# Kernel tuning notes

Hardware: AMD Instinct MI355X
Metric: run time of the kernel (lower is better)

The kernel has to match this reference:

```python
import jax, jax.numpy as jnp
import numpy as np

B, N, DA, DB = 8, 2048, 768, 1024


def setup_inputs() -> dict:
    key = jax.random.key(0)
    ks = jax.random.split(key, 20)
    s = 0.02
    inp = {
        "x_a": jax.random.normal(ks[0], (B, N, DA), jnp.float32),
        "x_b": jax.random.normal(ks[1], (B, N, DB), jnp.float32),
        # self-attention params (all DB x DB), stored as [in, out]
        "sa_wq": jax.random.normal(ks[2], (DB, DB), jnp.float32) * s,
        "sa_bq": jnp.zeros((DB,), jnp.float32),
        "sa_wk": jax.random.normal(ks[3], (DB, DB), jnp.float32) * s,
        "sa_bk": jnp.zeros((DB,), jnp.float32),
        "sa_wv": jax.random.normal(ks[4], (DB, DB), jnp.float32) * s,
        "sa_bv": jnp.zeros((DB,), jnp.float32),
        "sa_wo": jax.random.normal(ks[5], (DB, DB), jnp.float32) * s,
        "sa_bo": jnp.zeros((DB,), jnp.float32),
        # cross-attention params: q maps DA->DB, rest DB->DB
        "ca_wq": jax.random.normal(ks[6], (DA, DB), jnp.float32) * s,
        "ca_bq": jnp.zeros((DB,), jnp.float32),
        "ca_wk": jax.random.normal(ks[7], (DB, DB), jnp.float32) * s,
        "ca_bk": jnp.zeros((DB,), jnp.float32),
        "ca_wv": jax.random.normal(ks[8], (DB, DB), jnp.float32) * s,
        "ca_bv": jnp.zeros((DB,), jnp.float32),
        "ca_wo": jax.random.normal(ks[9], (DB, DB), jnp.float32) * s,
        "ca_bo": jnp.zeros((DB,), jnp.float32),
    }
    return inp


def _attend(q, k, v, scale):
    # q: [B,Nq,D], k,v: [B,Nk,D]
    scores = jnp.einsum("bqd,bkd->bqk", q, k) / scale
    w = jax.nn.softmax(scores, axis=-1)
    return jnp.einsum("bqk,bkd->bqd", w, v)


def reference(x_a, x_b,
              sa_wq, sa_bq, sa_wk, sa_bk, sa_wv, sa_bv, sa_wo, sa_bo,
              ca_wq, ca_bq, ca_wk, ca_bk, ca_wv, ca_bv, ca_wo, ca_bo):
    # self-attention on x_b; scale = sqrt(embed_dim_b)
    q = x_b @ sa_wq + sa_bq
    k = x_b @ sa_wk + sa_bk
    v = x_b @ sa_wv + sa_bv
    sa_out = _attend(q, k, v, jnp.sqrt(jnp.float32(x_b.shape[-1]))) @ sa_wo + sa_bo
    x_b = x_b + sa_out
    # cross-attention: q from x_a, k/v from updated x_b; scale = sqrt(embed_dim_a)
    q = x_a @ ca_wq + ca_bq
    k = x_b @ ca_wk + ca_bk
    v = x_b @ ca_wv + ca_bv
    ca_out = _attend(q, k, v, jnp.sqrt(jnp.float32(x_a.shape[-1]))) @ ca_wo + ca_bo
    return x_b + ca_out
```

## Files before the change

kernel.cpp:

```cpp
#include <hip/hip_runtime.h>
#include <hip/hip_bf16.h>


#define AS1 __attribute__((address_space(1)))
#define AS3 __attribute__((address_space(3)))

typedef __attribute__((ext_vector_type(8))) short bf16x8;
typedef __attribute__((ext_vector_type(4))) float f32x4;

using bf = __hip_bfloat16;

__global__ __launch_bounds__(512, 1) void gemm256(
    const bf* __restrict__ A, const bf* __restrict__ BT,
    const float* __restrict__ bias, const float* __restrict__ biasB,
    const float* __restrict__ biasC,
    const float* __restrict__ resid32, const bf* __restrict__ resid16,
    bf* __restrict__ C16, bf* __restrict__ C16b, bf* __restrict__ C16c,
    float* __restrict__ C32,
    int M, int Nc, int K, float alpha,
    long sA, long sB, long sC, int tstore, int nseg)
{
    __shared__ __align__(16) char lds[131072];

    const int tid  = threadIdx.x;
    const int wave = tid >> 6;
    const int lane = tid & 63;
    const int wm = wave >> 2;
    const int wn = wave & 3;

    const int gx = gridDim.x, gy = gridDim.y;
    int wg = blockIdx.y * gx + blockIdx.x;
    const int nwg = gx * gy;
    if (!(nwg & 7)) wg = (wg & 7) * (nwg >> 3) + (wg >> 3);
    const int m0 = (wg / gx) * 256;
    const int n0 = (wg % gx) * 256;

    const long zC = (long)blockIdx.z * sC;
    A  += (long)blockIdx.z * sA;
    BT += (long)blockIdx.z * sB;

    const int fl = lane & 15, qd = lane >> 4;
    const long ldb = (long)K * 2;

    const int scn = (lane & 7) ^ (lane >> 3);
    const char* gA = (const char*)A  + (long)(m0 + (lane >> 3)) * ldb + scn * 16;
    const char* gB = (const char*)BT + (long)(n0 + (lane >> 3)) * ldb + scn * 16;

    auto stage = [&](int mat, int h, int t) {
        const char* g = (mat ? gB : gA) + (long)(h * 128 + wave * 8) * ldb + (long)t * 128;
        char* l = lds + (t & 1) * 65536 + mat * 32768 + h * 16384 + wave * 1024;
        __builtin_amdgcn_global_load_lds((const AS1 void*)g,            (AS3 void*)l,        16, 0, 0);
        __builtin_amdgcn_global_load_lds((const AS1 void*)(g + 64*ldb), (AS3 void*)(l + 8192), 16, 0, 0);
    };

    const int s0slot = qd ^ (fl & 7);
    const int so0 = s0slot * 16;
    const int so1 = (s0slot ^ 4) * 16;
    const char* AbH0 = lds + wm * 16384 + fl * 128 + so0;
    const char* AbH1 = lds + wm * 16384 + fl * 128 + so1;
    const char* BbH0 = lds + 32768 + (wn >> 1) * 16384 + (wn & 1) * 8192 + fl * 128 + so0;
    const char* BbH1 = lds + 32768 + (wn >> 1) * 16384 + (wn & 1) * 8192 + fl * 128 + so1;

    f32x4 acc[8][4];
#pragma unroll
    for (int i = 0; i < 8; ++i)
#pragma unroll
        for (int j = 0; j < 4; ++j)
            acc[i][j] = (f32x4){0.f, 0.f, 0.f, 0.f};

    bf16x8 aA[4][2], aB[4][2];
    bf16x8 bP[2][2], bN[2][2], bQ1[2][2];

#define RD_A(dst, SL, mq) { \
    const char* pa0_ = AbH0 + (SL) * 65536 + (mq) * 8192; \
    const char* pa1_ = AbH1 + (SL) * 65536 + (mq) * 8192; \
    _Pragma("unroll") for (int f_ = 0; f_ < 4; ++f_) { \
        dst[f_][0] = *(const bf16x8*)(pa0_ + f_ * 2048); \
        dst[f_][1] = *(const bf16x8*)(pa1_ + f_ * 2048); } }

#define RD_B(dst, SL, nq) { \
    const char* pb0_ = BbH0 + (SL) * 65536 + (nq) * 4096; \
    const char* pb1_ = BbH1 + (SL) * 65536 + (nq) * 4096; \
    _Pragma("unroll") for (int g_ = 0; g_ < 2; ++g_) { \
        dst[g_][0] = *(const bf16x8*)(pb0_ + g_ * 2048); \
        dst[g_][1] = *(const bf16x8*)(pb1_ + g_ * 2048); } }

#define MFMA_Q(AF, BF, mq, nq) { \
    __builtin_amdgcn_s_setprio(1); \
    _Pragma("unroll") for (int f_ = 0; f_ < 4; ++f_) \
    _Pragma("unroll") for (int g_ = 0; g_ < 2; ++g_) \
    _Pragma("unroll") for (int h_ = 0; h_ < 2; ++h_) \
        acc[(mq)*4+f_][(nq)*2+g_] = __builtin_amdgcn_mfma_f32_16x16x32_bf16( \
            AF[f_][h_], BF[g_][h_], acc[(mq)*4+f_][(nq)*2+g_], 0, 0, 0); \
    __builtin_amdgcn_s_setprio(0); }

#define BAR() __builtin_amdgcn_s_barrier()
#define VMC(N) asm volatile("s_waitcnt vmcnt(" #N ")" ::: "memory")

    const int NT    = K >> 6;
    const int niter = NT >> 1;

#pragma unroll
    for (int t = 0; t < 2; ++t) {
        stage(0, 0, t); stage(1, 0, t); stage(0, 1, t); stage(1, 1, t);
    }
    VMC(6);
    BAR();
    RD_A(aA, 0, 0);

    for (int I = 0; I < niter; ++I) {
        const int t2a = 2 * I + 2, t2b = 2 * I + 3;
        const bool sa = t2a < NT;
        RD_B(bP, 0, 0); RD_B(bQ1, 0, 1);
        if (sa) stage(0, 0, t2a);
        BAR(); MFMA_Q(aA, bP, 0, 0); BAR();
        RD_A(aB, 0, 1);
        if (sa) stage(1, 0, t2a);
        BAR(); MFMA_Q(aA, bQ1, 0, 1); BAR();
        RD_A(aA, 1, 0);
        if (sa) stage(0, 1, t2a);
        BAR(); MFMA_Q(aB, bQ1, 1, 1); BAR();
        if (sa) { stage(1, 1, t2a); VMC(6); } else { VMC(0); }
        BAR(); MFMA_Q(aB, bP, 1, 0); BAR();
        RD_B(bN, 1, 0); RD_B(bQ1, 1, 1);
        if (sa) stage(0, 0, t2b);
        BAR(); MFMA_Q(aA, bN, 0, 0); BAR();
        RD_A(aB, 1, 1);
        if (sa) stage(1, 0, t2b);
        BAR(); MFMA_Q(aA, bQ1, 0, 1); BAR();
        if (sa) { RD_A(aA, 0, 0); stage(0, 1, t2b); }
        BAR(); MFMA_Q(aB, bQ1, 1, 1); BAR();
        if (sa) { stage(1, 1, t2b); VMC(6); }
        BAR(); MFMA_Q(aB, bN, 1, 0); BAR();
    }

    if (nseg == 1) {
        const long ldc = Nc;
#pragma unroll
        for (int i = 0; i < 8; ++i) {
#pragma unroll
            for (int j = 0; j < 4; ++j) {
#pragma unroll
                for (int r = 0; r < 4; ++r) {
                    const int row = m0 + wm * 128 + i * 16 + qd * 4 + r;
                    const int col = n0 + wn * 64 + j * 16 + fl;
                    float v = acc[i][j][r] * alpha;
                    if (bias) v += bias[col];
                    if (tstore & 1) {
                        const long idx = (long)(row >> 11) * ((long)Nc * 2048)
                                       + (long)col * 2048 + (row & 2047);
                        C16[idx] = __float2bfloat16(v);
                    } else {
                        const long idx = zC + (long)row * ldc + col;
                        if (resid32) v += resid32[idx];
                        if (resid16) v += __bfloat162float(resid16[idx]);
                        if (C16) C16[idx] = __float2bfloat16(v);
                        if (C32) C32[idx] = v;
                    }
                }
            }
        }
    } else {
        const int seg = n0 >> 10;
        bf* dst = (seg == 0) ? C16 : ((seg == 1) ? C16b : C16c);
        const float* bseg = (seg == 0) ? bias : ((seg == 1) ? biasB : biasC);
        const int trans = (tstore >> seg) & 1;
        const int cb = n0 & 1023;
#pragma unroll
        for (int i = 0; i < 8; ++i) {
#pragma unroll
            for (int j = 0; j < 4; ++j) {
#pragma unroll
                for (int r = 0; r < 4; ++r) {
                    const int row = m0 + wm * 128 + i * 16 + qd * 4 + r;
                    const int col = cb + wn * 64 + j * 16 + fl;
                    float v = acc[i][j][r] * alpha + bseg[col];
                    const long idx = trans
                        ? (long)(row >> 11) * (1024L * 2048) + (long)col * 2048 + (row & 2047)
                        : (long)row * 1024 + col;
                    dst[idx] = __float2bfloat16(v);
                }
            }
        }
    }
#undef RD_A
#undef RD_B
#undef MFMA_Q
#undef BAR
#undef VMC
}

__global__ __launch_bounds__(256) void cast_f32_bf16(
    const float* __restrict__ in, bf* __restrict__ out, long n)
{
    long i = ((long)blockIdx.x * 256 + threadIdx.x) * 8;
    if (i >= n) return;
    float4 a = *(const float4*)(in + i);
    float4 b = *(const float4*)(in + i + 4);
    bf o[8] = {__float2bfloat16(a.x), __float2bfloat16(a.y),
               __float2bfloat16(a.z), __float2bfloat16(a.w),
               __float2bfloat16(b.x), __float2bfloat16(b.y),
               __float2bfloat16(b.z), __float2bfloat16(b.w)};
    *(bf16x8*)(out + i) = *(bf16x8*)o;
}

__global__ __launch_bounds__(256) void transpose_f32_bf16(
    const float* __restrict__ in, bf* __restrict__ out, int R, int C)
{
    __shared__ bf t[32][33];
    const int c0 = blockIdx.x * 32, r0 = blockIdx.y * 32;
    const int tx = threadIdx.x, ty = threadIdx.y;
#pragma unroll
    for (int i = ty; i < 32; i += 8)
        t[i][tx] = __float2bfloat16(in[(long)(r0 + i) * C + c0 + tx]);
    __syncthreads();
#pragma unroll
    for (int i = ty; i < 32; i += 8)
        out[(long)(c0 + i) * R + r0 + tx] = t[tx][i];
}

__global__ __launch_bounds__(256) void softmax_rows(bf* __restrict__ S)
{
    const long row = blockIdx.x;
    bf* p = S + row * 2048;
    const int tx = threadIdx.x;

    float v[8];
    float m = -3.0e38f;
#pragma unroll
    for (int i = 0; i < 8; i++) {
        v[i] = __bfloat162float(p[tx + 256 * i]);
        m = fmaxf(m, v[i]);
    }
    __shared__ float red[4];
#pragma unroll
    for (int o = 1; o < 64; o <<= 1) m = fmaxf(m, __shfl_xor(m, o, 64));
    if ((tx & 63) == 0) red[tx >> 6] = m;
    __syncthreads();
    m = fmaxf(fmaxf(red[0], red[1]), fmaxf(red[2], red[3]));

    float s = 0.f;
#pragma unroll
    for (int i = 0; i < 8; i++) { v[i] = __expf(v[i] - m); s += v[i]; }
#pragma unroll
    for (int o = 1; o < 64; o <<= 1) s += __shfl_xor(s, o, 64);
    __syncthreads();
    if ((tx & 63) == 0) red[tx >> 6] = s;
    __syncthreads();
    const float inv = 1.0f / (red[0] + red[1] + red[2] + red[3]);
#pragma unroll
    for (int i = 0; i < 8; i++) p[tx + 256 * i] = __float2bfloat16(v[i] * inv);
}

extern "C" void kernel_launch(void* const* d_in, const int* in_sizes, int n_in,
                              void* d_out, int out_size, void* d_ws, size_t ws_size,
                              hipStream_t stream)
{
    const int Bb = 8, Nn = 2048, DA = 768, DB = 1024;
    const long Mt = (long)Bb * Nn;

    const float* x_a   = (const float*)d_in[0];
    const float* x_b   = (const float*)d_in[1];
    const float* sa_wq = (const float*)d_in[2];  const float* sa_bq = (const float*)d_in[3];
    const float* sa_wk = (const float*)d_in[4];  const float* sa_bk = (const float*)d_in[5];
    const float* sa_wv = (const float*)d_in[6];  const float* sa_bv = (const float*)d_in[7];
    const float* sa_wo = (const float*)d_in[8];  const float* sa_bo = (const float*)d_in[9];
    const float* ca_wq = (const float*)d_in[10]; const float* ca_bq = (const float*)d_in[11];
    const float* ca_wk = (const float*)d_in[12]; const float* ca_bk = (const float*)d_in[13];
    const float* ca_wv = (const float*)d_in[14]; const float* ca_bv = (const float*)d_in[15];
    const float* ca_wo = (const float*)d_in[16]; const float* ca_bo = (const float*)d_in[17];
    float* out = (float*)d_out;
    (void)in_sizes; (void)n_in; (void)out_size; (void)ws_size;

    char* ws = (char*)d_ws;
    size_t off = 0;
    auto alloc = [&](size_t bytes) -> bf* {
        bf* p = (bf*)(ws + off);
        off += (bytes + 255) & ~(size_t)255;
        return p;
    };
    bf* wqkvT = alloc((size_t)3 * DB * DB * 2);
    bf* woT   = alloc((size_t)DB * DB * 2);
    bf* cwqT  = alloc((size_t)DB * DA * 2);
    bf* ckvT  = alloc((size_t)2 * DB * DB * 2);
    bf* cwoT  = alloc((size_t)DB * DB * 2);
    bf* slA   = alloc((size_t)Mt * DB * 2);
    bf* slQ   = alloc((size_t)Mt * DB * 2);
    bf* slK   = alloc((size_t)Mt * DB * 2);
    bf* slV   = alloc((size_t)Mt * DB * 2);
    bf* S     = alloc((size_t)Bb * Nn * Nn * 2);

    const dim3 tb(32, 8);
    const dim3 blk(256);
    const dim3 blk5(512);
    const long sQ = (long)Nn * DB;
    const long sS = (long)Nn * Nn;
    const float* nf = nullptr;
    const bf*    nb = nullptr;
    bf*          no = nullptr;

    transpose_f32_bf16<<<dim3(DB/32, DB/32), tb, 0, stream>>>(sa_wq, wqkvT,                 DB, DB);
    transpose_f32_bf16<<<dim3(DB/32, DB/32), tb, 0, stream>>>(sa_wk, wqkvT + (size_t)DB*DB, DB, DB);
    transpose_f32_bf16<<<dim3(DB/32, DB/32), tb, 0, stream>>>(sa_wv, wqkvT + (size_t)2*DB*DB, DB, DB);
    transpose_f32_bf16<<<dim3(DB/32, DB/32), tb, 0, stream>>>(sa_wo, woT,  DB, DB);
    transpose_f32_bf16<<<dim3(DB/32, DA/32), tb, 0, stream>>>(ca_wq, cwqT, DA, DB);
    transpose_f32_bf16<<<dim3(DB/32, DB/32), tb, 0, stream>>>(ca_wk, ckvT,                 DB, DB);
    transpose_f32_bf16<<<dim3(DB/32, DB/32), tb, 0, stream>>>(ca_wv, ckvT + (size_t)DB*DB, DB, DB);
    transpose_f32_bf16<<<dim3(DB/32, DB/32), tb, 0, stream>>>(ca_wo, cwoT, DB, DB);

    cast_f32_bf16<<<dim3((unsigned)(Mt * DB / 8 / 256)), blk, 0, stream>>>(x_b, slA, Mt * DB);
    gemm256<<<dim3(3*DB/256, Mt/256, 1), blk5, 0, stream>>>(
        slA, wqkvT, sa_bq, sa_bk, sa_bv, nf, nb, slQ, slK, slV, nullptr,
        (int)Mt, 3*DB, DB, 1.0f, 0, 0, 0, 0b100, 3);
    gemm256<<<dim3(Nn/256, Nn/256, Bb), blk5, 0, stream>>>(
        slQ, slK, nf, nf, nf, nf, nb, S, no, no, nullptr,
        Nn, Nn, DB, 0.03125f, sQ, sQ, sS, 0, 1);
    softmax_rows<<<dim3((unsigned)(Bb * Nn)), blk, 0, stream>>>(S);
    gemm256<<<dim3(DB/256, Nn/256, Bb), blk5, 0, stream>>>(
        S, slV, nf, nf, nf, nf, nb, slK, no, no, nullptr,
        Nn, DB, Nn, 1.0f, sS, sQ, sQ, 0, 1);
    gemm256<<<dim3(DB/256, Mt/256, 1), blk5, 0, stream>>>(
        slK, woT, sa_bo, nf, nf, x_b, nb, slQ, no, no, nullptr,
        (int)Mt, DB, DB, 1.0f, 0, 0, 0, 0, 1);

    cast_f32_bf16<<<dim3((unsigned)(Mt * DA / 8 / 256)), blk, 0, stream>>>(x_a, slA, Mt * DA);
    gemm256<<<dim3(DB/256, Mt/256, 1), blk5, 0, stream>>>(
        slA, cwqT, ca_bq, nf, nf, nf, nb, slK, no, no, nullptr,
        (int)Mt, DB, DA, 1.0f, 0, 0, 0, 0, 1);
    gemm256<<<dim3(2*DB/256, Mt/256, 1), blk5, 0, stream>>>(
        slQ, ckvT, ca_bk, ca_bv, nf, nf, nb, slV, slA, no, nullptr,
        (int)Mt, 2*DB, DB, 1.0f, 0, 0, 0, 0b10, 2);
    gemm256<<<dim3(Nn/256, Nn/256, Bb), blk5, 0, stream>>>(
        slK, slV, nf, nf, nf, nf, nb, S, no, no, nullptr,
        Nn, Nn, DB, 0.036084391824351615f, sQ, sQ, sS, 0, 1);
    softmax_rows<<<dim3((unsigned)(Bb * Nn)), blk, 0, stream>>>(S);
    gemm256<<<dim3(DB/256, Nn/256, Bb), blk5, 0, stream>>>(
        S, slA, nf, nf, nf, nf, nb, slV, no, no, nullptr,
        Nn, DB, Nn, 1.0f, sS, sQ, sQ, 0, 1);
    gemm256<<<dim3(DB/256, Mt/256, 1), blk5, 0, stream>>>(
        slV, cwoT, ca_bo, nf, nf, nf, slQ, no, no, no, out,
        (int)Mt, DB, DB, 1.0f, 0, 0, 0, 0, 1);
}
```

Measured before the change: 1.109 ms.

## Reschedule GEMM prefetch staging order and waitcnt depth in main loop

Reorders the global-to-LDS stage calls within the double-buffered GEMM main loop so B-tiles and A-tiles are issued at different MFMA phases. The vmcnt wait depth is deepened from 6 to 8 outstanding loads, and the separate bN register buffer is removed by reusing bP. The goal is to overlap global loads with MFMA work more evenly and cut register pressure. The cost is a more delicate ordering of barriers and waitcnts, which could expose LDS hazards if the counts are wrong.

```diff
diff --git a/kernel.cpp b/kernel.cpp
--- a/kernel.cpp
+++ b/kernel.cpp
@@ -69,7 +69,7 @@
             acc[i][j] = (f32x4){0.f, 0.f, 0.f, 0.f};
 
     bf16x8 aA[4][2], aB[4][2];
-    bf16x8 bP[2][2], bN[2][2], bQ1[2][2];
+    bf16x8 bP[2][2], bQ1[2][2];
 
 #define RD_A(dst, SL, mq) { \
     const char* pa0_ = AbH0 + (SL) * 65536 + (mq) * 8192; \
@@ -102,36 +102,40 @@
 
 #pragma unroll
     for (int t = 0; t < 2; ++t) {
-        stage(0, 0, t); stage(1, 0, t); stage(0, 1, t); stage(1, 1, t);
+        stage(1, 0, t); stage(1, 1, t); stage(0, 0, t); stage(0, 1, t);
     }
-    VMC(6);
+    VMC(8);
     BAR();
     RD_A(aA, 0, 0);
 
     for (int I = 0; I < niter; ++I) {
-        const int t2a = 2 * I + 2, t2b = 2 * I + 3;
-        const bool sa = t2a < NT;
+        const int n0t = 2 * I + 2, n1t = 2 * I + 3;
+        const bool sa = n0t < NT;
         RD_B(bP, 0, 0); RD_B(bQ1, 0, 1);
-        if (sa) stage(0, 0, t2a);
         BAR(); MFMA_Q(aA, bP, 0, 0); BAR();
         RD_A(aB, 0, 1);
-        if (sa) stage(1, 0, t2a);
+        if (sa) stage(1, 0, n0t);
         BAR(); MFMA_Q(aA, bQ1, 0, 1); BAR();
+        if (sa) { stage(1, 1, n0t); stage(0, 0, n0t); }
+        BAR(); MFMA_Q(aB, bQ1, 1, 1); BAR();
+        if (sa) { stage(0, 1, n0t); VMC(8); } else { VMC(0); }
+        BAR();
         RD_A(aA, 1, 0);
-        if (sa) stage(0, 1, t2a);
+        MFMA_Q(aB, bP, 1, 0); BAR();
+        RD_B(bP, 1, 0); RD_B(bQ1, 1, 1);
+        BAR(); MFMA_Q(aA, bP, 0, 0); BAR();
+        RD_A(aB, 1, 1);
+        if (sa) stage(1, 0, n1t);
+        BAR(); MFMA_Q(aA, bQ1, 0, 1); BAR();
+        if (sa) { stage(1, 1, n1t); stage(0, 0, n1t); }
         BAR(); MFMA_Q(aB, bQ1, 1, 1); BAR();
-        if (sa) { stage(1, 1, t2a); VMC(6); } else { VMC(0); }
-        BAR(); MFMA_Q(aB, bP, 1, 0); BAR();
-        RD_B(bN, 1, 0); RD_B(bQ1, 1, 1);
-        if (sa) stage(0, 0, t2b);
-        BAR(); MFMA_Q(aA, bN, 0, 0); BAR();
-        RD_A(aB, 1, 1);
-        if (sa) stage(1, 0, t2b);
-        BAR(); MFMA_Q(aA, bQ1, 0, 1); BAR();
-        if (sa) { RD_A(aA, 0, 0); stage(0, 1, t2b); }
-        BAR(); MFMA_Q(aB, bQ1, 1, 1); BAR();
-        if (sa) { stage(1, 1, t2b); VMC(6); }
-        BAR(); MFMA_Q(aB, bN, 1, 0); BAR();
+        if (sa) {
+            stage(0, 1, n1t); VMC(8); BAR();
+            RD_A(aA, 0, 0);
+        } else {
+            BAR();
+        }
+        MFMA_Q(aB, bP, 1, 0); BAR();
     }
 
     if (nseg == 1) {
```

Measured after the change: 1.149 ms. 3.6% more time.
